# Kernel tuning notes

Measured on AMD Instinct MI355X. Metric: run time of the kernel, lower is better.

Reference implementation:

```python
import jax, jax.numpy as jnp
import numpy as np

EPS = 1e-6


def setup_inputs() -> dict:
    key = jax.random.key(0)
    kx, ky = jax.random.split(key)
    B, T, N, D = 2, 16, 1024, 3
    x = jax.random.normal(kx, (B, T, N, D), dtype=jnp.float32)
    y = jax.random.normal(ky, (B, T, N, D), dtype=jnp.float32)
    return {"x": x, "y": y}


def reference(x, y):
    B, T, N, _ = x.shape
    xf = x.reshape(B * T, N, -1)  # (BT, N, 3)
    yf = y.reshape(B * T, N, -1)  # (BT, N, 3)
    # Squared pairwise distances via norms + cross term to avoid the
    # (BT, N, N, 3) diff tensor; index i runs over y, j over x, matching
    # dist[b, i, j] = ||x[b, j] - y[b, i]||^2 in the torch code.
    x2 = jnp.sum(xf * xf, axis=-1)               # (BT, N)
    y2 = jnp.sum(yf * yf, axis=-1)               # (BT, N)
    cross = jnp.einsum("bid,bjd->bij", yf, xf)   # (BT, N, N)
    sq = jnp.maximum(y2[:, :, None] + x2[:, None, :] - 2.0 * cross, 0.0)
    dist = jnp.sqrt(EPS + sq)                    # (BT, N, N)
    min1 = jnp.min(dist, axis=1)  # nearest y for each x point -> (BT, N)
    min2 = jnp.min(dist, axis=2)  # nearest x for each y point -> (BT, N)
    return jnp.mean(min1) + jnp.mean(min2)
```

## Files before the change

kernel.cpp:

```cpp
#include <hip/hip_runtime.h>
#include <math.h>

#define EPSF 1e-6f
#define N_PTS 1024
#define BT 32
#define RC 16
#define CHUNK 64

__global__ __launch_bounds__(128) void chamfer_stage(
    const float* __restrict__ x, const float* __restrict__ y,
    float* __restrict__ ws) {
  const int t   = threadIdx.x;
  const int rc  = blockIdx.x;
  const int b   = blockIdx.y;
  const int dir = blockIdx.z;

  const float* qarr = dir ? y : x;
  const float* rarr = dir ? x : y;
  const float* qb = qarr + (size_t)b * (N_PTS * 3);
  const float* rb = rarr + (size_t)b * (N_PTS * 3) + (size_t)rc * (CHUNK * 3);

  __shared__ float4 s[CHUNK];
  if (t < CHUNK) {
    const float rx = rb[t * 3 + 0];
    const float ry = rb[t * 3 + 1];
    const float rz = rb[t * 3 + 2];
    s[t] = make_float4(-2.0f * rx, -2.0f * ry, -2.0f * rz,
                       rx * rx + ry * ry + rz * rz);
  }
  __syncthreads();

  float qx[8], qy[8], qz[8], q2[8], m[8];
#pragma unroll
  for (int k = 0; k < 8; ++k) {
    const int j = t + 128 * k;
    qx[k] = qb[j * 3 + 0];
    qy[k] = qb[j * 3 + 1];
    qz[k] = qb[j * 3 + 2];
    q2[k] = qx[k] * qx[k] + qy[k] * qy[k] + qz[k] * qz[k];
    m[k] = 3.4e38f;
  }

#pragma unroll 4
  for (int i = 0; i < CHUNK; i += 2) {
    const float4 r0 = s[i];
    const float4 r1 = s[i + 1];
#pragma unroll
    for (int k = 0; k < 8; ++k) {
      float v0 = fmaf(qx[k], r0.x, r0.w);
      v0 = fmaf(qy[k], r0.y, v0);
      v0 = fmaf(qz[k], r0.z, v0);
      float v1 = fmaf(qx[k], r1.x, r1.w);
      v1 = fmaf(qy[k], r1.y, v1);
      v1 = fmaf(qz[k], r1.z, v1);
      m[k] = fminf(m[k], fminf(v0, v1));
    }
  }

  float* wbase = ws + ((size_t)(dir * BT + b) * RC + rc) * N_PTS;
#pragma unroll
  for (int k = 0; k < 8; ++k) {
    const int j = t + 128 * k;
    wbase[j] = fmaxf(q2[k] + m[k], 0.0f);
  }
}

__global__ __launch_bounds__(256) void chamfer_reduce(
    const float* __restrict__ ws, float* __restrict__ out) {
  const int g = blockIdx.x * 256 + threadIdx.x;
  const float2* base = (const float2*)ws + g;
  float2 mn = base[0];
#pragma unroll
  for (int r = 1; r < RC; ++r) {
    const float2 v = base[(size_t)r * (N_PTS / 2) * (2 * BT / RC) * (RC / (2 * BT)) ];
    (void)v; break;
  }
  {
    const int dirb = g >> 9;
    const int qp = g & 511;
    const float2* p = (const float2*)ws + (size_t)dirb * RC * 512 + qp;
    mn = p[0];
#pragma unroll
    for (int r = 1; r < RC; ++r) {
      const float2 v = p[(size_t)r * 512];
      mn.x = fminf(mn.x, v.x);
      mn.y = fminf(mn.y, v.y);
    }
  }
  float d = sqrtf(EPSF + mn.x) + sqrtf(EPSF + mn.y);

  for (int off = 32; off > 0; off >>= 1) d += __shfl_down(d, off, 64);

  __shared__ float wsum[4];
  if ((threadIdx.x & 63) == 0) wsum[threadIdx.x >> 6] = d;
  __syncthreads();
  if (threadIdx.x == 0) {
    atomicAdd(out, (wsum[0] + wsum[1] + wsum[2] + wsum[3]) * (1.0f / 32768.0f));
  }
}

__global__ __launch_bounds__(256) void chamfer_simple(
    const float* __restrict__ x, const float* __restrict__ y,
    float* __restrict__ out) {
  const int t   = threadIdx.x;
  const int qc  = blockIdx.x;
  const int b   = blockIdx.y;
  const int dir = blockIdx.z;

  const float* qarr = dir ? y : x;
  const float* rarr = dir ? x : y;
  const float* qb = qarr + (size_t)b * N_PTS * 3;
  const float* rb = rarr + (size_t)b * N_PTS * 3;

  __shared__ float4 s[N_PTS];
  for (int i = t; i < N_PTS; i += 256) {
    const float rx = rb[i * 3], ry = rb[i * 3 + 1], rz = rb[i * 3 + 2];
    s[i] = make_float4(-2.0f * rx, -2.0f * ry, -2.0f * rz,
                       rx * rx + ry * ry + rz * rz);
  }
  __syncthreads();

  const int j = qc * 256 + t;
  const float qx = qb[j * 3], qy = qb[j * 3 + 1], qz = qb[j * 3 + 2];
  const float q2 = qx * qx + qy * qy + qz * qz;
  float m = 3.4e38f;
#pragma unroll 8
  for (int i = 0; i < N_PTS; i += 2) {
    const float4 r0 = s[i];
    const float4 r1 = s[i + 1];
    float v0 = fmaf(qx, r0.x, r0.w);
    v0 = fmaf(qy, r0.y, v0);
    v0 = fmaf(qz, r0.z, v0);
    float v1 = fmaf(qx, r1.x, r1.w);
    v1 = fmaf(qy, r1.y, v1);
    v1 = fmaf(qz, r1.z, v1);
    m = fminf(m, fminf(v0, v1));
  }
  float d = sqrtf(EPSF + fmaxf(q2 + m, 0.0f));

  for (int off = 32; off > 0; off >>= 1) d += __shfl_down(d, off, 64);

  __shared__ float wsum[4];
  if ((t & 63) == 0) wsum[t >> 6] = d;
  __syncthreads();
  if (t == 0) {
    atomicAdd(out, (wsum[0] + wsum[1] + wsum[2] + wsum[3]) * (1.0f / 32768.0f));
  }
}

extern "C" void kernel_launch(void* const* d_in, const int* in_sizes, int n_in,
                              void* d_out, int out_size, void* d_ws, size_t ws_size,
                              hipStream_t stream) {
  const float* x = (const float*)d_in[0];
  const float* y = (const float*)d_in[1];
  float* out = (float*)d_out;

  hipMemsetAsync(out, 0, sizeof(float) * out_size, stream);

  const size_t ws_need = (size_t)2 * BT * RC * N_PTS * sizeof(float);
  if (ws_size >= ws_need) {
    chamfer_stage<<<dim3(RC, BT, 2), 128, 0, stream>>>(x, y, (float*)d_ws);
    chamfer_reduce<<<dim3(128), 256, 0, stream>>>((const float*)d_ws, out);
  } else {
    chamfer_simple<<<dim3(4, BT, 2), 256, 0, stream>>>(x, y, out);
  }
}
```

Before: 67.15 us.

## Fuse two-stage chamfer into single kernel with in-block reference split

Replaces the stage kernel plus workspace-based min-reduction kernel with one fused kernel. Each block takes 256 query points and loads all 1024 reference points into shared memory. Each wavefront scans a quarter of the references for 4 query points per lane, and the partial minima are combined through shared memory before the sqrt and sum. This removes a kernel launch and the global workspace round-trip, at the cost of fewer blocks (256 vs 1024) and fewer queries held per thread.

```diff
diff --git a/kernel.cpp b/kernel.cpp
--- a/kernel.cpp
+++ b/kernel.cpp
@@ -4,49 +4,57 @@
 #define EPSF 1e-6f
 #define N_PTS 1024
 #define BT 32
-#define RC 16
-#define CHUNK 64
+#define QB 256
+#define RCHUNK 256
 
-__global__ __launch_bounds__(128) void chamfer_stage(
+__global__ __launch_bounds__(256) void chamfer_fused(
     const float* __restrict__ x, const float* __restrict__ y,
-    float* __restrict__ ws) {
+    float* __restrict__ out) {
   const int t   = threadIdx.x;
-  const int rc  = blockIdx.x;
+  const int w   = t >> 6;
+  const int l   = t & 63;
+  const int qc  = blockIdx.x;
   const int b   = blockIdx.y;
   const int dir = blockIdx.z;
 
   const float* qarr = dir ? y : x;
   const float* rarr = dir ? x : y;
-  const float* qb = qarr + (size_t)b * (N_PTS * 3);
-  const float* rb = rarr + (size_t)b * (N_PTS * 3) + (size_t)rc * (CHUNK * 3);
+  const float* qb = qarr + (size_t)b * (N_PTS * 3) + (size_t)qc * (QB * 3);
+  const float* rb = rarr + (size_t)b * (N_PTS * 3);
 
-  __shared__ float4 s[CHUNK];
-  if (t < CHUNK) {
-    const float rx = rb[t * 3 + 0];
-    const float ry = rb[t * 3 + 1];
-    const float rz = rb[t * 3 + 2];
-    s[t] = make_float4(-2.0f * rx, -2.0f * ry, -2.0f * rz,
+  __shared__ float4 s[N_PTS];
+  __shared__ float pmin[4][QB];
+  __shared__ float wsum[4];
+
+#pragma unroll
+  for (int r = 0; r < 4; ++r) {
+    const int i = t + 256 * r;
+    const float rx = rb[i * 3 + 0];
+    const float ry = rb[i * 3 + 1];
+    const float rz = rb[i * 3 + 2];
+    s[i] = make_float4(-2.0f * rx, -2.0f * ry, -2.0f * rz,
                        rx * rx + ry * ry + rz * rz);
   }
-  __syncthreads();
 
-  float qx[8], qy[8], qz[8], q2[8], m[8];
+  float qx[4], qy[4], qz[4], q2[4], m[4];
 #pragma unroll
-  for (int k = 0; k < 8; ++k) {
-    const int j = t + 128 * k;
+  for (int k = 0; k < 4; ++k) {
+    const int j = l + 64 * k;
     qx[k] = qb[j * 3 + 0];
     qy[k] = qb[j * 3 + 1];
     qz[k] = qb[j * 3 + 2];
     q2[k] = qx[k] * qx[k] + qy[k] * qy[k] + qz[k] * qz[k];
     m[k] = 3.4e38f;
   }
+  __syncthreads();
 
+  const float4* sc = s + w * RCHUNK;
 #pragma unroll 4
-  for (int i = 0; i < CHUNK; i += 2) {
-    const float4 r0 = s[i];
-    const float4 r1 = s[i + 1];
+  for (int i = 0; i < RCHUNK; i += 2) {
+    const float4 r0 = sc[i];
+    const float4 r1 = sc[i + 1];
 #pragma unroll
-    for (int k = 0; k < 8; ++k) {
+    for (int k = 0; k < 4; ++k) {
       float v0 = fmaf(qx[k], r0.x, r0.w);
       v0 = fmaf(qy[k], r0.y, v0);
       v0 = fmaf(qz[k], r0.z, v0);
@@ -57,94 +65,20 @@
     }
   }
 
-  float* wbase = ws + ((size_t)(dir * BT + b) * RC + rc) * N_PTS;
 #pragma unroll
-  for (int k = 0; k < 8; ++k) {
-    const int j = t + 128 * k;
-    wbase[j] = fmaxf(q2[k] + m[k], 0.0f);
-  }
-}
+  for (int k = 0; k < 4; ++k) pmin[w][l + 64 * k] = q2[k] + m[k];
+  __syncthreads();
 
-__global__ __launch_bounds__(256) void chamfer_reduce(
-    const float* __restrict__ ws, float* __restrict__ out) {
-  const int g = blockIdx.x * 256 + threadIdx.x;
-  const float2* base = (const float2*)ws + g;
-  float2 mn = base[0];
-#pragma unroll
-  for (int r = 1; r < RC; ++r) {
-    const float2 v = base[(size_t)r * (N_PTS / 2) * (2 * BT / RC) * (RC / (2 * BT)) ];
-    (void)v; break;
-  }
-  {
-    const int dirb = g >> 9;
-    const int qp = g & 511;
-    const float2* p = (const float2*)ws + (size_t)dirb * RC * 512 + qp;
-    mn = p[0];
-#pragma unroll
-    for (int r = 1; r < RC; ++r) {
-      const float2 v = p[(size_t)r * 512];
-      mn.x = fminf(mn.x, v.x);
-      mn.y = fminf(mn.y, v.y);
-    }
-  }
-  float d = sqrtf(EPSF + mn.x) + sqrtf(EPSF + mn.y);
+  const float v = fminf(fminf(pmin[0][t], pmin[1][t]),
+                        fminf(pmin[2][t], pmin[3][t]));
+  float d = sqrtf(EPSF + fmaxf(v, 0.0f));
 
   for (int off = 32; off > 0; off >>= 1) d += __shfl_down(d, off, 64);
-
-  __shared__ float wsum[4];
-  if ((threadIdx.x & 63) == 0) wsum[threadIdx.x >> 6] = d;
-  __syncthreads();
-  if (threadIdx.x == 0) {
-    atomicAdd(out, (wsum[0] + wsum[1] + wsum[2] + wsum[3]) * (1.0f / 32768.0f));
-  }
-}
-
-__global__ __launch_bounds__(256) void chamfer_simple(
-    const float* __restrict__ x, const float* __restrict__ y,
-    float* __restrict__ out) {
-  const int t   = threadIdx.x;
-  const int qc  = blockIdx.x;
-  const int b   = blockIdx.y;
-  const int dir = blockIdx.z;
-
-  const float* qarr = dir ? y : x;
-  const float* rarr = dir ? x : y;
-  const float* qb = qarr + (size_t)b * N_PTS * 3;
-  const float* rb = rarr + (size_t)b * N_PTS * 3;
-
-  __shared__ float4 s[N_PTS];
-  for (int i = t; i < N_PTS; i += 256) {
-    const float rx = rb[i * 3], ry = rb[i * 3 + 1], rz = rb[i * 3 + 2];
-    s[i] = make_float4(-2.0f * rx, -2.0f * ry, -2.0f * rz,
-                       rx * rx + ry * ry + rz * rz);
-  }
-  __syncthreads();
-
-  const int j = qc * 256 + t;
-  const float qx = qb[j * 3], qy = qb[j * 3 + 1], qz = qb[j * 3 + 2];
-  const float q2 = qx * qx + qy * qy + qz * qz;
-  float m = 3.4e38f;
-#pragma unroll 8
-  for (int i = 0; i < N_PTS; i += 2) {
-    const float4 r0 = s[i];
-    const float4 r1 = s[i + 1];
-    float v0 = fmaf(qx, r0.x, r0.w);
-    v0 = fmaf(qy, r0.y, v0);
-    v0 = fmaf(qz, r0.z, v0);
-    float v1 = fmaf(qx, r1.x, r1.w);
-    v1 = fmaf(qy, r1.y, v1);
-    v1 = fmaf(qz, r1.z, v1);
-    m = fminf(m, fminf(v0, v1));
-  }
-  float d = sqrtf(EPSF + fmaxf(q2 + m, 0.0f));
-
-  for (int off = 32; off > 0; off >>= 1) d += __shfl_down(d, off, 64);
-
-  __shared__ float wsum[4];
-  if ((t & 63) == 0) wsum[t >> 6] = d;
+  if (l == 0) wsum[w] = d;
   __syncthreads();
   if (t == 0) {
-    atomicAdd(out, (wsum[0] + wsum[1] + wsum[2] + wsum[3]) * (1.0f / 32768.0f));
+    atomicAdd(out, (wsum[0] + wsum[1] + wsum[2] + wsum[3]) *
+                       (1.0f / 32768.0f));
   }
 }
 
@@ -157,11 +91,5 @@
 
   hipMemsetAsync(out, 0, sizeof(float) * out_size, stream);
 
-  const size_t ws_need = (size_t)2 * BT * RC * N_PTS * sizeof(float);
-  if (ws_size >= ws_need) {
-    chamfer_stage<<<dim3(RC, BT, 2), 128, 0, stream>>>(x, y, (float*)d_ws);
-    chamfer_reduce<<<dim3(128), 256, 0, stream>>>((const float*)d_ws, out);
-  } else {
-    chamfer_simple<<<dim3(4, BT, 2), 256, 0, stream>>>(x, y, out);
-  }
+  chamfer_fused<<<dim3(4, BT, 2), 256, 0, stream>>>(x, y, out);
 }
```

After: 70.05 us. 4.3% more time.
